# Kernel tuning notes

Measured on AMD Instinct MI355X. Metric: run time of the kernel, lower is better.

Reference implementation:

```python
import jax, jax.numpy as jnp
import numpy as np

S, B, D = 2048, 2, 1024
H, DH = 16, 64  # heads, dim_head; H*DH == D (required by out.view)
SCALE = DH ** -0.5


def setup_inputs() -> dict:
    key = jax.random.key(0)
    ks = jax.random.split(key, 9)
    s = 0.02
    return {
        "x": jax.random.normal(ks[0], (S, B, D), jnp.float32),
        "Wq": jax.random.normal(ks[1], (H * DH, D), jnp.float32) * s,
        "bq": jax.random.normal(ks[2], (H * DH,), jnp.float32) * s,
        "Wk": jax.random.normal(ks[3], (H * DH, D), jnp.float32) * s,
        "bk": jax.random.normal(ks[4], (H * DH,), jnp.float32) * s,
        "Wv": jax.random.normal(ks[5], (H * DH, D), jnp.float32) * s,
        "bv": jax.random.normal(ks[6], (H * DH,), jnp.float32) * s,
        "Wo": jax.random.normal(ks[7], (D, H * DH), jnp.float32) * s,
        "bo": jax.random.normal(ks[8], (D,), jnp.float32) * s,
    }


def reference(x, Wq, bq, Wk, bk, Wv, bv, Wo, bo):
    # x: [S, B, D] (seq-first, matching the torch module)
    q = (x @ Wq.T + bq).reshape(S, B, H, DH)
    k = (x @ Wk.T + bk).reshape(S, B, H, DH)
    v = (x @ Wv.T + bv).reshape(S, B, H, DH)
    # scores: [B, H, S, S]
    dots = jnp.einsum("sbhd,tbhd->bhst", q, k) * SCALE
    attn = jax.nn.softmax(dots, axis=-1)  # dropout p=0.0 -> identity
    out = jnp.einsum("bhst,tbhd->sbhd", attn, v).reshape(S, B, H * DH)
    return out @ Wo.T + bo
```

## Files before the change

### kernel.cpp

```cpp
#include <hip/hip_runtime.h>
#include <hip/hip_bf16.h>

typedef unsigned short u16;
typedef unsigned int u32;
typedef __bf16 bf16x8 __attribute__((ext_vector_type(8)));
typedef float f32x4 __attribute__((ext_vector_type(4)));
typedef float f32x16 __attribute__((ext_vector_type(16)));

static constexpr int kS = 2048;
static constexpr int kB = 2;
static constexpr int kD = 1024;
static constexpr int kDH = 64;
static constexpr int kM = kS * kB;
static constexpr float kScale = 0.125f;
static constexpr float kLog2e = 1.44269504088896340736f;

__device__ __forceinline__ u16 f2bf(float f) {
  return __builtin_bit_cast(u16, static_cast<__bf16>(f));
}

__device__ __forceinline__ u32 pack2(float lo, float hi) {
  union { u16 h[2]; u32 u; } x;
  x.h[0] = f2bf(lo); x.h[1] = f2bf(hi);
  return x.u;
}

__device__ __forceinline__ void permswap(u32& a, u32& b) {
  asm volatile("v_permlane32_swap_b32 %0, %1" : "+v"(a), "+v"(b));
}

__device__ __forceinline__ float exp2_hw(float x) {
  float r;
  asm("v_exp_f32 %0, %1" : "=v"(r) : "v"(x));
  return r;
}

__device__ __forceinline__ void load_lds16(const void* g, void* l) {
  __builtin_amdgcn_global_load_lds(
      (const __attribute__((address_space(1))) void*)g,
      (__attribute__((address_space(3))) void*)l, 16, 0, 0);
}

__global__ void cast_all(const float* __restrict__ x,
                         const float* __restrict__ Wq, const float* __restrict__ Wk,
                         const float* __restrict__ Wv, const float* __restrict__ Wo,
                         u16* __restrict__ xb,
                         u16* __restrict__ dq, u16* __restrict__ dk,
                         u16* __restrict__ dv, u16* __restrict__ dw) {
  const int bid = blockIdx.x;
  const float* src; u16* dst; int i;
  if (bid < 4096) {
    src = x; dst = xb;
    i = (bid * 256 + (int)threadIdx.x) * 4;
  } else {
    const int r = bid - 4096;
    switch (r >> 10) {
      case 0: src = Wq; dst = dq; break;
      case 1: src = Wk; dst = dk; break;
      case 2: src = Wv; dst = dv; break;
      default: src = Wo; dst = dw; break;
    }
    i = ((r & 1023) * 256 + (int)threadIdx.x) * 4;
  }
  const float4 v = *reinterpret_cast<const float4*>(src + i);
  ushort4 o;
  o.x = f2bf(v.x); o.y = f2bf(v.y); o.z = f2bf(v.z); o.w = f2bf(v.w);
  *reinterpret_cast<ushort4*>(dst + i) = o;
}

template <int MODE>
__device__ __forceinline__ void gemm_body(
    const u16* __restrict__ A, const u16* __restrict__ W,
    const float* __restrict__ bias, void* __restrict__ Out,
    int M, int N, int K, float oscale) {
  __shared__ u16 As[128 * 64];
  __shared__ u16 Bs[128 * 64];
  const int tid = threadIdx.x;
  const int lane = tid & 63;
  const int wid = tid >> 6;
  const int wr = (wid >> 2) * 64;
  const int wc = (wid & 3) * 32;
  const int l15 = lane & 15;
  const int lg = lane >> 4;
  const int tm = blockIdx.x * 128;
  const int tn = blockIdx.y * 128;

  auto stage = [&](int k0) {
#pragma unroll
    for (int p = 0; p < 2; ++p) {
      const int c = p * 512 + tid;
      const int row = c >> 3;
      const int scc = (c & 7) ^ (row & 7);
      load_lds16(A + (size_t)(tm + row) * K + k0 + scc * 8, &As[c * 8]);
      load_lds16(W + (size_t)(tn + row) * K + k0 + scc * 8, &Bs[c * 8]);
    }
  };

  f32x4 acc[4][2] = {};

#pragma unroll 1
  for (int ks = 0; ks < K / 64; ++ks) {
    stage(ks * 64);
    __syncthreads();
#pragma unroll
    for (int kh = 0; kh < 2; ++kh) {
      bf16x8 af[4], bw[2];
#pragma unroll
      for (int i = 0; i < 4; ++i) {
        const int row = wr + i * 16 + l15;
        af[i] = *reinterpret_cast<const bf16x8*>(
            &As[row * 64 + (((kh * 4 + lg) ^ (row & 7)) * 8)]);
      }
#pragma unroll
      for (int j = 0; j < 2; ++j) {
        const int row = wc + j * 16 + l15;
        bw[j] = *reinterpret_cast<const bf16x8*>(
            &Bs[row * 64 + (((kh * 4 + lg) ^ (row & 7)) * 8)]);
      }
#pragma unroll
      for (int i = 0; i < 4; ++i)
#pragma unroll
        for (int j = 0; j < 2; ++j)
          acc[i][j] = __builtin_amdgcn_mfma_f32_16x16x32_bf16(af[i], bw[j], acc[i][j], 0, 0, 0);
    }
    __syncthreads();
  }

#pragma unroll
  for (int i = 0; i < 4; ++i)
#pragma unroll
    for (int j = 0; j < 2; ++j)
#pragma unroll
      for (int r = 0; r < 4; ++r) {
        const int row = tm + wr + i * 16 + lg * 4 + r;
        const int col = tn + wc + j * 16 + l15;
        const float v = (acc[i][j][r] + bias[col]) * oscale;
        if constexpr (MODE == 0) {
          reinterpret_cast<u16*>(Out)[(size_t)row * N + col] = f2bf(v);
        } else {
          const int s_ = row >> 1, b_ = row & 1;
          const int h_ = col >> 6, dh_ = col & 63;
          reinterpret_cast<u16*>(Out)[((size_t)(b_ * 16 + h_) * 64 + dh_) * kS + s_] = f2bf(v);
        }
      }
}

__global__ __launch_bounds__(512, 6) void qkv_gemm(
    const u16* __restrict__ xb,
    const u16* __restrict__ Wqb, const u16* __restrict__ Wkb, const u16* __restrict__ Wvb,
    const float* __restrict__ bq, const float* __restrict__ bk, const float* __restrict__ bv,
    u16* __restrict__ Q, u16* __restrict__ K, u16* __restrict__ Vt) {
  const int z = blockIdx.z;
  if (z == 2) {
    gemm_body<2>(xb, Wvb, bv, Vt, kM, kD, kD, 1.0f);
  } else if (z == 0) {
    gemm_body<0>(xb, Wqb, bq, Q, kM, kD, kD, kScale * kLog2e);
  } else {
    gemm_body<0>(xb, Wkb, bk, K, kM, kD, kD, 1.0f);
  }
}

__global__ __launch_bounds__(512, 4) void out_gemm(
    const u16* __restrict__ A, const u16* __restrict__ W,
    const float* __restrict__ bias, float* __restrict__ Out) {
  __shared__ u16 As[128 * 64];
  __shared__ u16 Bs[64 * 64];
  const int tid = threadIdx.x;
  const int lane = tid & 63;
  const int wid = tid >> 6;
  const int wr = (wid >> 1) * 32;
  const int wc = (wid & 1) * 32;
  const int l15 = lane & 15;
  const int lg = lane >> 4;
  const int tm = blockIdx.x * 128;
  const int tn = blockIdx.y * 64;
  const int K = kD, N = kD;

  auto stage = [&](int k0) {
#pragma unroll
    for (int p = 0; p < 3; ++p) {
      const int c = p * 512 + tid;
      if (c < 1024) {
        const int row = c >> 3;
        const int scc = (c & 7) ^ (row & 7);
        load_lds16(A + (size_t)(tm + row) * K + k0 + scc * 8, &As[c * 8]);
      } else {
        const int cb = c - 1024;
        const int row = cb >> 3;
        const int scc = (cb & 7) ^ (row & 7);
        load_lds16(W + (size_t)(tn + row) * K + k0 + scc * 8, &Bs[cb * 8]);
      }
    }
  };

  f32x4 acc[2][2] = {};

#pragma unroll 1
  for (int ks = 0; ks < K / 64; ++ks) {
    stage(ks * 64);
    __syncthreads();
#pragma unroll
    for (int kh = 0; kh < 2; ++kh) {
      bf16x8 af[2], bw[2];
#pragma unroll
      for (int i = 0; i < 2; ++i) {
        const int row = wr + i * 16 + l15;
        af[i] = *reinterpret_cast<const bf16x8*>(
            &As[row * 64 + (((kh * 4 + lg) ^ (row & 7)) * 8)]);
      }
#pragma unroll
      for (int j = 0; j < 2; ++j) {
        const int row = wc + j * 16 + l15;
        bw[j] = *reinterpret_cast<const bf16x8*>(
            &Bs[row * 64 + (((kh * 4 + lg) ^ (row & 7)) * 8)]);
      }
#pragma unroll
      for (int i = 0; i < 2; ++i)
#pragma unroll
        for (int j = 0; j < 2; ++j)
          acc[i][j] = __builtin_amdgcn_mfma_f32_16x16x32_bf16(af[i], bw[j], acc[i][j], 0, 0, 0);
    }
    __syncthreads();
  }

#pragma unroll
  for (int i = 0; i < 2; ++i)
#pragma unroll
    for (int j = 0; j < 2; ++j)
#pragma unroll
      for (int r = 0; r < 4; ++r) {
        const int row = tm + wr + i * 16 + lg * 4 + r;
        const int col = tn + wc + j * 16 + l15;
        Out[(size_t)row * N + col] = acc[i][j][r] + bias[col];
      }
}

__global__ __launch_bounds__(512, 4) void attn_fwd(
    const u16* __restrict__ Qg, const u16* __restrict__ Kg,
    const u16* __restrict__ Vtg, u16* __restrict__ Og) {
  __shared__ u16 Ksm[2 * 4096];
  __shared__ u16 Vsm[2 * 2 * 4096];

  const int tid = threadIdx.x;
  const int lane = tid & 63;
  const int w = tid >> 6;
  const int half = w >> 2;
  const int wsub = w & 3;
  const int ltid = tid & 255;
  const int l31 = lane & 31;
  const int hi = lane >> 5;

  const int bid = blockIdx.x;
  const int xcd = bid & 7;
  const int idx = bid >> 3;
  const int bh = xcd * 4 + (idx & 3);
  const int qb = idx >> 2;
  const int b = bh & 1;
  const int h = bh >> 1;
  const int hoff = h * kDH;
  const int vslot = b * 16 + h;
  const int qrow = qb * 128 + wsub * 32 + l31;

  u16* Kh = &Ksm[half * 4096];
  u16* Vh = &Vsm[half * 2 * 4096];

  bf16x8 qf[4];
#pragma unroll
  for (int ks = 0; ks < 4; ++ks)
    qf[ks] = *reinterpret_cast<const bf16x8*>(
        &Qg[(size_t)(qrow * kB + b) * kD + hoff + ks * 16 + hi * 8]);

  f32x16 acc[2] = {};
  float lac[4] = {0.f, 0.f, 0.f, 0.f};

  auto stage = [&](int t0, int vbuf) {
#pragma unroll
    for (int p = 0; p < 2; ++p) {
      const int c = p * 256 + ltid;
      const int row = c >> 3;
      const int scc = (c & 7) ^ (row & 7);
      load_lds16(&Kg[(size_t)((t0 + row) * kB + b) * kD + hoff + scc * 8],
                 &Kh[c * 8]);
      load_lds16(&Vtg[(size_t)(vslot * 64 + row) * kS + t0 + scc * 8],
                 &Vh[vbuf * 4096 + c * 8]);
    }
  };

  const int tbase = half * 16;
  stage(tbase * 64, 0);

#pragma unroll 1
  for (int ti = 0; ti < 16; ++ti) {
    asm volatile("s_waitcnt vmcnt(0)" ::: "memory");
    __builtin_amdgcn_sched_barrier(0);
    __builtin_amdgcn_s_barrier();
    __builtin_amdgcn_sched_barrier(0);

    f32x16 sc[2] = {};
    __builtin_amdgcn_s_setprio(1);
#pragma unroll
    for (int nb = 0; nb < 2; ++nb) {
      const int krow = nb * 32 + l31;
#pragma unroll
      for (int ks = 0; ks < 4; ++ks) {
        const bf16x8 kf = *reinterpret_cast<const bf16x8*>(
            &Kh[krow * 64 + (((ks * 2 + hi) ^ (krow & 7)) * 8)]);
        sc[nb] = __builtin_amdgcn_mfma_f32_32x32x16_bf16(kf, qf[ks], sc[nb], 0, 0, 0);
      }
    }
    __builtin_amdgcn_s_setprio(0);

    __builtin_amdgcn_sched_barrier(0);
    __builtin_amdgcn_s_barrier();
    __builtin_amdgcn_sched_barrier(0);
    if (ti + 1 < 16) stage((tbase + ti + 1) * 64, (ti + 1) & 1);

    const int cur = ti & 1;

    bf16x8 pb[4];
#pragma unroll
    for (int nb = 0; nb < 2; ++nb) {
      float p[16];
#pragma unroll
      for (int r = 0; r < 16; ++r) {
        p[r] = exp2_hw(sc[nb][r]);
        lac[r & 3] += p[r];
      }
      u32 pk[4][2];
#pragma unroll
      for (int q = 0; q < 4; ++q)
#pragma unroll
        for (int w2 = 0; w2 < 2; ++w2)
          pk[q][w2] = pack2(p[4 * q + 2 * w2], p[4 * q + 2 * w2 + 1]);
#pragma unroll
      for (int k1 = 0; k1 < 2; ++k1) {
        u32 a0 = pk[2 * k1][0], b0 = pk[2 * k1 + 1][0];
        u32 a1 = pk[2 * k1][1], b1 = pk[2 * k1 + 1][1];
        permswap(a0, b0);
        permswap(a1, b1);
        union { u32 wv[4]; bf16x8 v; } U;
        U.wv[0] = a0; U.wv[1] = a1; U.wv[2] = b0; U.wv[3] = b1;
        pb[2 * nb + k1] = U.v;
      }
    }

    __builtin_amdgcn_s_setprio(1);
#pragma unroll
    for (int ks = 0; ks < 4; ++ks)
#pragma unroll
      for (int n2 = 0; n2 < 2; ++n2) {
        const int vrow = n2 * 32 + l31;
        const bf16x8 va = *reinterpret_cast<const bf16x8*>(
            &Vh[cur * 4096 + vrow * 64 + (((ks * 2 + hi) ^ (vrow & 7)) * 8)]);
        acc[n2] = __builtin_amdgcn_mfma_f32_32x32x16_bf16(va, pb[ks], acc[n2], 0, 0, 0);
      }
    __builtin_amdgcn_s_setprio(0);
  }

  __syncthreads();
  float* Ocmb = reinterpret_cast<float*>(&Vsm[0]);
  float* Lcmb = reinterpret_cast<float*>(&Ksm[0]);
  const float l_own = (lac[0] + lac[1]) + (lac[2] + lac[3]);
  const float l_half = l_own + __shfl_xor(l_own, 32);
  const int q = wsub * 32 + l31;

  if (half == 1) {
    if (hi == 0) Lcmb[q] = l_half;
#pragma unroll
    for (int n2 = 0; n2 < 2; ++n2)
#pragma unroll
      for (int q4 = 0; q4 < 4; ++q4)
#pragma unroll
        for (int rp = 0; rp < 2; ++rp) {
          const int dh0 = n2 * 32 + q4 * 8 + hi * 4 + rp * 2;
          const int a = q * 64 + (dh0 ^ ((l31 & 7) << 3));
          *reinterpret_cast<float2*>(&Ocmb[a]) =
              make_float2(acc[n2][q4 * 4 + rp * 2], acc[n2][q4 * 4 + rp * 2 + 1]);
        }
  }
  __syncthreads();
  if (half == 0) {
    const float inv = 1.0f / (l_half + Lcmb[q]);
#pragma unroll
    for (int n2 = 0; n2 < 2; ++n2)
#pragma unroll
      for (int q4 = 0; q4 < 4; ++q4)
#pragma unroll
        for (int rp = 0; rp < 2; ++rp) {
          const int dh0 = n2 * 32 + q4 * 8 + hi * 4 + rp * 2;
          const int a = q * 64 + (dh0 ^ ((l31 & 7) << 3));
          const float2 o = *reinterpret_cast<const float2*>(&Ocmb[a]);
          acc[n2][q4 * 4 + rp * 2]     += o.x;
          acc[n2][q4 * 4 + rp * 2 + 1] += o.y;
        }
#pragma unroll
    for (int n2 = 0; n2 < 2; ++n2)
#pragma unroll
      for (int g = 0; g < 4; ++g) {
        const int dh0 = n2 * 32 + g * 8 + hi * 4;
        ushort4 o;
        o.x = f2bf(acc[n2][g * 4 + 0] * inv);
        o.y = f2bf(acc[n2][g * 4 + 1] * inv);
        o.z = f2bf(acc[n2][g * 4 + 2] * inv);
        o.w = f2bf(acc[n2][g * 4 + 3] * inv);
        *reinterpret_cast<ushort4*>(&Og[(size_t)(qrow * kB + b) * kD + hoff + dh0]) = o;
      }
  }
}

extern "C" void kernel_launch(void* const* d_in, const int* in_sizes, int n_in,
                              void* d_out, int out_size, void* d_ws, size_t ws_size,
                              hipStream_t stream) {
  const float* x  = (const float*)d_in[0];
  const float* Wq = (const float*)d_in[1];
  const float* bq = (const float*)d_in[2];
  const float* Wk = (const float*)d_in[3];
  const float* bk = (const float*)d_in[4];
  const float* Wv = (const float*)d_in[5];
  const float* bv = (const float*)d_in[6];
  const float* Wo = (const float*)d_in[7];
  const float* bo = (const float*)d_in[8];
  float* out = (float*)d_out;

  char* ws = (char*)d_ws;
  u16* xb  = (u16*)(ws + 0);
  u16* Wqb = (u16*)(ws + 8388608);
  u16* Wkb = (u16*)(ws + 10485760);
  u16* Wvb = (u16*)(ws + 12582912);
  u16* Wob = (u16*)(ws + 14680064);
  u16* Qb  = (u16*)(ws + 16777216);
  u16* Kb  = (u16*)(ws + 25165824);
  u16* Vtb = (u16*)(ws + 33554432);
  u16* Ob  = (u16*)(ws + 41943040);

  cast_all<<<8192, 256, 0, stream>>>(x, Wq, Wk, Wv, Wo, xb, Wqb, Wkb, Wvb, Wob);

  qkv_gemm<<<dim3(kM / 128, kD / 128, 3), 512, 0, stream>>>(
      xb, Wqb, Wkb, Wvb, bq, bk, bv, Qb, Kb, Vtb);

  attn_fwd<<<512, 512, 0, stream>>>(Qb, Kb, Vtb, Ob);

  out_gemm<<<dim3(kM / 128, kD / 64), 512, 0, stream>>>(Ob, Wob, bo, out);
}
```

Baseline: 111.9 us.

## Double-buffer LDS tiles in QKV and output GEMMs to overlap loads with MFMA

Both GEMM kernels now use two LDS buffers. The next K-slice is prefetched into the alternate buffer while MFMAs run on the current one, and each iteration uses one wait plus barrier instead of two __syncthreads. The intent is to hide global-to-LDS load latency behind compute. This doubles LDS use per block, and the QKV kernel's launch bounds drop from 6 to 4 blocks per CU, which may reduce occupancy.

After: 111.3 us. About the same (-0.6%).

```diff
diff --git a/kernel.cpp b/kernel.cpp
--- a/kernel.cpp
+++ b/kernel.cpp
@@ -69,12 +69,11 @@
 }
 
 template <int MODE>
-__device__ __forceinline__ void gemm_body(
+__device__ __forceinline__ void gemm_big(
+    u16* __restrict__ AsB, u16* __restrict__ BsB,
     const u16* __restrict__ A, const u16* __restrict__ W,
     const float* __restrict__ bias, void* __restrict__ Out,
     int M, int N, int K, float oscale) {
-  __shared__ u16 As[128 * 64];
-  __shared__ u16 Bs[128 * 64];
   const int tid = threadIdx.x;
   const int lane = tid & 63;
   const int wid = tid >> 6;
@@ -85,23 +84,39 @@
   const int tm = blockIdx.x * 128;
   const int tn = blockIdx.y * 128;
 
-  auto stage = [&](int k0) {
-#pragma unroll
-    for (int p = 0; p < 2; ++p) {
+  auto stage = [&](int k0, int buf) {
+#pragma unroll
+    for (int p = 0; p < 4; ++p) {
       const int c = p * 512 + tid;
-      const int row = c >> 3;
-      const int scc = (c & 7) ^ (row & 7);
-      load_lds16(A + (size_t)(tm + row) * K + k0 + scc * 8, &As[c * 8]);
-      load_lds16(W + (size_t)(tn + row) * K + k0 + scc * 8, &Bs[c * 8]);
+      if (c < 1024) {
+        const int row = c >> 3;
+        const int scc = (c & 7) ^ (row & 7);
+        load_lds16(A + (size_t)(tm + row) * K + k0 + scc * 8, &AsB[buf * 8192 + c * 8]);
+      } else {
+        const int cb = c - 1024;
+        const int row = cb >> 3;
+        const int scc = (cb & 7) ^ (row & 7);
+        load_lds16(W + (size_t)(tn + row) * K + k0 + scc * 8, &BsB[buf * 8192 + cb * 8]);
+      }
     }
   };
 
   f32x4 acc[4][2] = {};
+  const int nsteps = K / 64;
+
+  stage(0, 0);
 
 #pragma unroll 1
-  for (int ks = 0; ks < K / 64; ++ks) {
-    stage(ks * 64);
-    __syncthreads();
+  for (int ks = 0; ks < nsteps; ++ks) {
+    asm volatile("s_waitcnt vmcnt(0)" ::: "memory");
+    __builtin_amdgcn_sched_barrier(0);
+    __builtin_amdgcn_s_barrier();
+    __builtin_amdgcn_sched_barrier(0);
+    const int cur = ks & 1;
+    if (ks + 1 < nsteps) stage((ks + 1) * 64, cur ^ 1);
+
+    const u16* as = &AsB[cur * 8192];
+    const u16* bs = &BsB[cur * 8192];
 #pragma unroll
     for (int kh = 0; kh < 2; ++kh) {
       bf16x8 af[4], bw[2];
@@ -109,13 +124,13 @@
       for (int i = 0; i < 4; ++i) {
         const int row = wr + i * 16 + l15;
         af[i] = *reinterpret_cast<const bf16x8*>(
-            &As[row * 64 + (((kh * 4 + lg) ^ (row & 7)) * 8)]);
+            &as[row * 64 + (((kh * 4 + lg) ^ (row & 7)) * 8)]);
       }
 #pragma unroll
       for (int j = 0; j < 2; ++j) {
         const int row = wc + j * 16 + l15;
         bw[j] = *reinterpret_cast<const bf16x8*>(
-            &Bs[row * 64 + (((kh * 4 + lg) ^ (row & 7)) * 8)]);
+            &bs[row * 64 + (((kh * 4 + lg) ^ (row & 7)) * 8)]);
       }
 #pragma unroll
       for (int i = 0; i < 4; ++i)
@@ -123,7 +138,6 @@
         for (int j = 0; j < 2; ++j)
           acc[i][j] = __builtin_amdgcn_mfma_f32_16x16x32_bf16(af[i], bw[j], acc[i][j], 0, 0, 0);
     }
-    __syncthreads();
   }
 
 #pragma unroll
@@ -145,26 +159,28 @@
       }
 }
 
-__global__ __launch_bounds__(512, 6) void qkv_gemm(
+__global__ __launch_bounds__(512, 4) void qkv_gemm(
     const u16* __restrict__ xb,
     const u16* __restrict__ Wqb, const u16* __restrict__ Wkb, const u16* __restrict__ Wvb,
     const float* __restrict__ bq, const float* __restrict__ bk, const float* __restrict__ bv,
     u16* __restrict__ Q, u16* __restrict__ K, u16* __restrict__ Vt) {
+  __shared__ u16 As[2 * 128 * 64];
+  __shared__ u16 Bs[2 * 128 * 64];
   const int z = blockIdx.z;
   if (z == 2) {
-    gemm_body<2>(xb, Wvb, bv, Vt, kM, kD, kD, 1.0f);
+    gemm_big<2>(As, Bs, xb, Wvb, bv, Vt, kM, kD, kD, 1.0f);
   } else if (z == 0) {
-    gemm_body<0>(xb, Wqb, bq, Q, kM, kD, kD, kScale * kLog2e);
+    gemm_big<0>(As, Bs, xb, Wqb, bq, Q, kM, kD, kD, kScale * kLog2e);
   } else {
-    gemm_body<0>(xb, Wkb, bk, K, kM, kD, kD, 1.0f);
+    gemm_big<0>(As, Bs, xb, Wkb, bk, K, kM, kD, kD, 1.0f);
   }
 }
 
 __global__ __launch_bounds__(512, 4) void out_gemm(
     const u16* __restrict__ A, const u16* __restrict__ W,
     const float* __restrict__ bias, float* __restrict__ Out) {
-  __shared__ u16 As[128 * 64];
-  __shared__ u16 Bs[64 * 64];
+  __shared__ u16 As[2 * 128 * 64];
+  __shared__ u16 Bs[2 * 64 * 64];
   const int tid = threadIdx.x;
   const int lane = tid & 63;
   const int wid = tid >> 6;
@@ -176,29 +192,39 @@
   const int tn = blockIdx.y * 64;
   const int K = kD, N = kD;
 
-  auto stage = [&](int k0) {
+  auto stage = [&](int k0, int buf) {
 #pragma unroll
     for (int p = 0; p < 3; ++p) {
       const int c = p * 512 + tid;
       if (c < 1024) {
         const int row = c >> 3;
         const int scc = (c & 7) ^ (row & 7);
-        load_lds16(A + (size_t)(tm + row) * K + k0 + scc * 8, &As[c * 8]);
+        load_lds16(A + (size_t)(tm + row) * K + k0 + scc * 8, &As[buf * 8192 + c * 8]);
       } else {
         const int cb = c - 1024;
         const int row = cb >> 3;
         const int scc = (cb & 7) ^ (row & 7);
-        load_lds16(W + (size_t)(tn + row) * K + k0 + scc * 8, &Bs[cb * 8]);
+        load_lds16(W + (size_t)(tn + row) * K + k0 + scc * 8, &Bs[buf * 4096 + cb * 8]);
       }
     }
   };
 
   f32x4 acc[2][2] = {};
+  const int nsteps = K / 64;
+
+  stage(0, 0);
 
 #pragma unroll 1
-  for (int ks = 0; ks < K / 64; ++ks) {
-    stage(ks * 64);
-    __syncthreads();
+  for (int ks = 0; ks < nsteps; ++ks) {
+    asm volatile("s_waitcnt vmcnt(0)" ::: "memory");
+    __builtin_amdgcn_sched_barrier(0);
+    __builtin_amdgcn_s_barrier();
+    __builtin_amdgcn_sched_barrier(0);
+    const int cur = ks & 1;
+    if (ks + 1 < nsteps) stage((ks + 1) * 64, cur ^ 1);
+
+    const u16* as = &As[cur * 8192];
+    const u16* bs = &Bs[cur * 4096];
 #pragma unroll
     for (int kh = 0; kh < 2; ++kh) {
       bf16x8 af[2], bw[2];
@@ -206,13 +232,13 @@
       for (int i = 0; i < 2; ++i) {
         const int row = wr + i * 16 + l15;
         af[i] = *reinterpret_cast<const bf16x8*>(
-            &As[row * 64 + (((kh * 4 + lg) ^ (row & 7)) * 8)]);
+            &as[row * 64 + (((kh * 4 + lg) ^ (row & 7)) * 8)]);
       }
 #pragma unroll
       for (int j = 0; j < 2; ++j) {
         const int row = wc + j * 16 + l15;
         bw[j] = *reinterpret_cast<const bf16x8*>(
-            &Bs[row * 64 + (((kh * 4 + lg) ^ (row & 7)) * 8)]);
+            &bs[row * 64 + (((kh * 4 + lg) ^ (row & 7)) * 8)]);
       }
 #pragma unroll
       for (int i = 0; i < 2; ++i)
@@ -220,7 +246,6 @@
         for (int j = 0; j < 2; ++j)
           acc[i][j] = __builtin_amdgcn_mfma_f32_16x16x32_bf16(af[i], bw[j], acc[i][j], 0, 0, 0);
     }
-    __syncthreads();
   }
 
 #pragma unroll
```
